# Kernel optimization log

Measured on AMD Instinct MI355X. Metric: run time of the kernel, lower is better.

## Reference

```python
import jax, jax.numpy as jnp
import numpy as np

N, E, F, H, G, C = 50000, 800000, 128, 128, 500, 10
L = 3  # num_conv_layers
EPS = 1e-5


def batch_norm(x, g, b):
    # training-mode BatchNorm1d: biased variance, eps=1e-5
    mu = jnp.mean(x, axis=0)
    var = jnp.var(x, axis=0)
    return (x - mu) * jax.lax.rsqrt(var + EPS) * g + b


def gcn_conv(x, W, bias, src, dst, n):
    # x' = D^{-1/2} (A + I) D^{-1/2} (x W) + bias, edge weights = 1
    xw = x @ W
    loop = jnp.arange(n)
    s = jnp.concatenate([src, loop])  # sources incl. self-loops
    d = jnp.concatenate([dst, loop])  # targets incl. self-loops
    w = jnp.ones(s.shape[0], x.dtype)
    deg = jax.ops.segment_sum(w, s, num_segments=n)
    dinv = jnp.where(deg > 0, jax.lax.rsqrt(deg), 0.0)
    norm = dinv[s] * w * dinv[d]
    msg = xw[s] * norm[:, None]  # gather + scale
    out = jax.ops.segment_sum(msg, d, num_segments=n)  # scatter-add
    return out + bias


def setup_inputs() -> dict:
    key = jax.random.key(0)
    ks = jax.random.split(key, 16)
    x = jax.random.normal(ks[0], (N, F), dtype=jnp.float32)
    edge_index = jax.random.randint(ks[1], (2, E), 0, N, dtype=jnp.int64)
    batch = jnp.sort(jax.random.randint(ks[2], (N,), 0, G, dtype=jnp.int64))
    sF = 1.0 / np.sqrt(F)
    sH = 1.0 / np.sqrt(H)
    return {
        "x": x,
        "edge_index": edge_index,
        "batch": batch,
        "bn_feat_g": jnp.ones((F,), jnp.float32),
        "bn_feat_b": jnp.full((F,), 1e-4, jnp.float32),
        "W_feat": jax.random.normal(ks[3], (F, H), jnp.float32) * sF,
        "bns_conv_g": jnp.ones((L, H), jnp.float32),
        "bns_conv_b": jnp.full((L, H), 1e-4, jnp.float32),
        "W_conv": jax.random.normal(ks[4], (L, H, H), jnp.float32) * sH,
        "b_conv": jnp.zeros((L, H), jnp.float32),
        "bn_fc_g": jnp.ones((H,), jnp.float32),
        "bn_fc_b": jnp.full((H,), 1e-4, jnp.float32),
        "W_lin": jax.random.normal(ks[5], (H, H), jnp.float32) * sH,
        "b_lin": jnp.zeros((H,), jnp.float32),
        "bn_hid_g": jnp.ones((H,), jnp.float32),
        "bn_hid_b": jnp.full((H,), 1e-4, jnp.float32),
        "W_cls": jax.random.normal(ks[6], (H, C), jnp.float32) * sH,
        "b_cls": jnp.zeros((C,), jnp.float32),
    }


def reference(x, edge_index, batch, bn_feat_g, bn_feat_b, W_feat,
              bns_conv_g, bns_conv_b, W_conv, b_conv,
              bn_fc_g, bn_fc_b, W_lin, b_lin,
              bn_hid_g, bn_hid_b, W_cls, b_cls):
    src, dst = edge_index[0], edge_index[1]
    h = batch_norm(x, bn_feat_g, bn_feat_b)
    h = jax.nn.relu(h @ W_feat)  # gfn conv: linear only, no bias/propagation
    for i in range(L):
        h = batch_norm(h, bns_conv_g[i], bns_conv_b[i])
        h = jax.nn.relu(gcn_conv(h, W_conv[i], b_conv[i], src, dst, N))
    h = jax.ops.segment_sum(h, batch, num_segments=G)  # global_add_pool
    h = batch_norm(h, bn_fc_g, bn_fc_b)
    h = jax.nn.relu(h @ W_lin + b_lin)
    h = batch_norm(h, bn_hid_g, bn_hid_b)
    logits = h @ W_cls + b_cls
    return jax.nn.log_softmax(logits, axis=-1)
```

## Files before the change

kernel.cpp:

```cpp
#include <hip/hip_runtime.h>

#define NF 128
#define EPS 1e-5f
#define KELL 64

typedef unsigned short ushort_t;
typedef unsigned int uint_t;

using bf16x8 = __attribute__((ext_vector_type(8))) short;
using f32x4  = __attribute__((ext_vector_type(4))) float;

static __device__ inline ushort_t f2bf(float f) {
    uint_t u = __float_as_uint(f);
    return (ushort_t)((u + 0x7fffu + ((u >> 16) & 1u)) >> 16);
}


__global__ void k_fill_ell(const int* __restrict__ ei, int* __restrict__ scnt,
                           int* __restrict__ dcnt, ushort_t* __restrict__ colx, int E) {
    int e = blockIdx.x * 256 + threadIdx.x;
    if (e < E) {
        int s = ei[e], d = ei[E + e];
        atomicAdd(&scnt[s], 1);
        int pos = atomicAdd(&dcnt[d], 1);
        if (pos < KELL - 1) colx[d * KELL + pos] = (ushort_t)s;
    }
}

__global__ void k_finish(const int* __restrict__ scnt, const int* __restrict__ dcnt,
                         float* __restrict__ dinv, ushort_t* __restrict__ colx,
                         ushort_t* __restrict__ BbSent, int n) {
    int i = blockIdx.x * 256 + threadIdx.x;
    if (i < n) {
        dinv[i] = rsqrtf((float)scnt[i] + 1.0f);
        int dc = min(dcnt[i], KELL - 1);
        ushort_t* row = colx + i * KELL;
        row[dc] = (ushort_t)i;
        int len = (dc + 16) & ~15;
        for (int q = dc + 1; q < len; ++q) row[q] = (ushort_t)n;
    }
    if (blockIdx.x == 0 && threadIdx.x < 64)
        ((uint_t*)BbSent)[threadIdx.x] = 0;
}


__global__ void bn_stats(const float* __restrict__ h, float* __restrict__ stats, int n) {
    int j = threadIdx.x & 127;
    int half = threadIdx.x >> 7;
    float s = 0.f, q = 0.f;
    for (int r = blockIdx.x * 2 + half; r < n; r += gridDim.x * 2) {
        float v = h[r * NF + j];
        s += v;
        q += v * v;
    }
    __shared__ float ls[256], lq[256];
    ls[threadIdx.x] = s; lq[threadIdx.x] = q;
    __syncthreads();
    if (threadIdx.x < 128) {
        atomicAdd(&stats[j], ls[threadIdx.x] + ls[threadIdx.x + 128]);
        atomicAdd(&stats[NF + j], lq[threadIdx.x] + lq[threadIdx.x + 128]);
    }
}


__global__ void pack_w4(const float* __restrict__ W0, const float* __restrict__ W123,
                        ushort_t* __restrict__ Wp) {
    int gidx = blockIdx.x * 256 + threadIdx.x;
    int mat = gidx >> 11, idx = gidx & 2047;
    const float* W = (mat == 0) ? W0 : (W123 + (size_t)(mat - 1) * NF * NF);
    int lane = idx & 63, ct = (idx >> 6) & 7, kc = idx >> 9;
    int m = lane & 15, q = lane >> 4;
    ushort_t o[8];
#pragma unroll
    for (int j = 0; j < 8; ++j)
        o[j] = f2bf(W[(kc * 32 + q * 8 + j) * NF + ct * 16 + m]);
    *(uint4*)&Wp[(size_t)gidx * 8] = *(uint4*)o;
}


#define HSTRIDE 136

__launch_bounds__(256)
__global__ void gemm_mfma(const float* __restrict__ Hh, const ushort_t* __restrict__ Wp,
                          const float* __restrict__ stats, const float* __restrict__ gW,
                          const float* __restrict__ bB, float inv_n,
                          const float* __restrict__ bias, const float* __restrict__ rowscale,
                          float* __restrict__ out, ushort_t* __restrict__ outb,
                          int nrows, int relu, int obf) {
    __shared__ ushort_t hs[64 * HSTRIDE];
    __shared__ float acs[256];
    const int tid = threadIdx.x;
    const int rb = blockIdx.x * 64;

    if (tid < 128) {
        float mean = stats[tid] * inv_n;
        float var = stats[NF + tid] * inv_n - mean * mean;
        float rstd = rsqrtf(var + EPS);
        float a = gW[tid] * rstd;
        acs[tid] = a;
        acs[NF + tid] = bB[tid] - mean * a;
    }
    __syncthreads();
    const float4* ac4 = (const float4*)acs;

#pragma unroll
    for (int p = 0; p < 8; ++p) {
        int idx = p * 256 + tid;
        int r = idx >> 5, k4 = idx & 31;
        int gr = rb + r;
        float4 v = (gr < nrows) ? *(const float4*)&Hh[(size_t)gr * NF + k4 * 4]
                                : make_float4(0.f, 0.f, 0.f, 0.f);
        float4 a4 = ac4[k4], c4 = ac4[32 + k4];
        ushort_t o[4];
        o[0] = f2bf(fmaf(v.x, a4.x, c4.x));
        o[1] = f2bf(fmaf(v.y, a4.y, c4.y));
        o[2] = f2bf(fmaf(v.z, a4.z, c4.z));
        o[3] = f2bf(fmaf(v.w, a4.w, c4.w));
        *(uint2*)&hs[r * HSTRIDE + k4 * 4] = *(uint2*)o;
    }
    __syncthreads();

    const int wave = tid >> 6, lane = tid & 63;
    const int m = lane & 15, q = lane >> 4;
    const ushort_t* arow = &hs[(wave * 16 + m) * HSTRIDE];

    f32x4 acc[8];
#pragma unroll
    for (int ct = 0; ct < 8; ++ct) acc[ct] = (f32x4){0.f, 0.f, 0.f, 0.f};

#pragma unroll
    for (int kc = 0; kc < 4; ++kc) {
        bf16x8 af = *(const bf16x8*)&arow[kc * 32 + q * 8];
        const ushort_t* wp = Wp + kc * 4096 + lane * 8;
#pragma unroll
        for (int ct = 0; ct < 8; ++ct) {
            bf16x8 bfr = *(const bf16x8*)&wp[ct * 512];
            acc[ct] = __builtin_amdgcn_mfma_f32_16x16x32_bf16(af, bfr, acc[ct], 0, 0, 0);
        }
    }

#pragma unroll
    for (int r = 0; r < 4; ++r) {
        int grow = rb + wave * 16 + q * 4 + r;
        if (grow < nrows) {
            float rs = (obf && rowscale) ? rowscale[grow] : 1.0f;
#pragma unroll
            for (int ct = 0; ct < 8; ++ct) {
                int col = ct * 16 + m;
                float v = acc[ct][r] + (bias ? bias[col] : 0.f);
                if (relu) v = fmaxf(v, 0.f);
                if (obf) outb[(size_t)grow * NF + col] = f2bf(v * rs);
                else     out[(size_t)grow * NF + col] = v;
            }
        }
    }
}


__launch_bounds__(256)
__global__ void gemm_bn(const float* __restrict__ Hh, const float* __restrict__ W,
                        const float* __restrict__ stats, const float* __restrict__ gW,
                        const float* __restrict__ bB, float inv_n,
                        const float* __restrict__ bias,
                        float* __restrict__ out, int nrows, int relu) {
    __shared__ float hsb[64][133];
    __shared__ float acs[256];
    const int tid = threadIdx.x;
    const int tx = tid & 15;
    const int ty = tid >> 4;
    const int rb = blockIdx.x * 64;

    if (tid < 128) {
        float mean = stats[tid] * inv_n;
        float var = stats[NF + tid] * inv_n - mean * mean;
        float rstd = rsqrtf(var + EPS);
        float a = gW[tid] * rstd;
        acs[tid] = a;
        acs[NF + tid] = bB[tid] - mean * a;
    }
    __syncthreads();

#pragma unroll 8
    for (int p = 0; p < 32; ++p) {
        int idx = p * 256 + tid;
        int r = idx >> 7, k = idx & 127;
        int gr = rb + r;
        float v = (gr < nrows) ? Hh[(size_t)gr * NF + k] : 0.f;
        hsb[r][k] = fmaf(v, acs[k], acs[NF + k]);
    }
    __syncthreads();

    float acc[4][8];
#pragma unroll
    for (int i = 0; i < 4; ++i)
#pragma unroll
        for (int j = 0; j < 8; ++j) acc[i][j] = 0.f;

    const int c0 = tx * 4, c1 = 64 + tx * 4;
#pragma unroll 4
    for (int k = 0; k < 128; ++k) {
        const float4 b0 = *(const float4*)&W[k * NF + c0];
        const float4 b1 = *(const float4*)&W[k * NF + c1];
#pragma unroll
        for (int i = 0; i < 4; ++i) {
            float a = hsb[ty * 4 + i][k];
            acc[i][0] = fmaf(a, b0.x, acc[i][0]);
            acc[i][1] = fmaf(a, b0.y, acc[i][1]);
            acc[i][2] = fmaf(a, b0.z, acc[i][2]);
            acc[i][3] = fmaf(a, b0.w, acc[i][3]);
            acc[i][4] = fmaf(a, b1.x, acc[i][4]);
            acc[i][5] = fmaf(a, b1.y, acc[i][5]);
            acc[i][6] = fmaf(a, b1.z, acc[i][6]);
            acc[i][7] = fmaf(a, b1.w, acc[i][7]);
        }
    }

#pragma unroll
    for (int i = 0; i < 4; ++i) {
        int gr = rb + ty * 4 + i;
        if (gr < nrows) {
            float o[8];
#pragma unroll
            for (int j = 0; j < 8; ++j) {
                int c = (j < 4) ? (c0 + j) : (c1 + j - 4);
                float v = acc[i][j] + (bias ? bias[c] : 0.f);
                o[j] = relu ? fmaxf(v, 0.f) : v;
            }
            *(float4*)&out[(size_t)gr * NF + c0] = make_float4(o[0], o[1], o[2], o[3]);
            *(float4*)&out[(size_t)gr * NF + c1] = make_float4(o[4], o[5], o[6], o[7]);
        }
    }
}


#define CVT2(u, a, b) { a = __uint_as_float((u) << 16); b = __uint_as_float((u) & 0xffff0000u); }
#define ACC8(q) { float p0, p1, p2, p3, p4, p5, p6, p7;                          \
    CVT2(q.x, p0, p1) CVT2(q.y, p2, p3) CVT2(q.z, p4, p5) CVT2(q.w, p6, p7)      \
    acc[0] += p0; acc[1] += p1; acc[2] += p2; acc[3] += p3;                      \
    acc[4] += p4; acc[5] += p5; acc[6] += p6; acc[7] += p7; }

__launch_bounds__(256)
__global__ void k_aggregate_bf(const ushort_t* __restrict__ xwb, const int* __restrict__ dcnt,
                               const ushort_t* __restrict__ colx, const float* __restrict__ dinv,
                               const float* __restrict__ bias, float* __restrict__ out, int n) {
    int node = blockIdx.x * 16 + (threadIdx.x >> 4);
    int lane = threadIdx.x & 15;
    if (node >= n) return;
    const uint4* __restrict__ xq = (const uint4*)xwb;
    float acc[8];
#pragma unroll
    for (int j = 0; j < 8; ++j) acc[j] = 0.f;
    int dc = min(dcnt[node], KELL - 1);
    int len = (dc + 16) & ~15;
    int e0 = node * KELL;
    for (int e = e0; e < e0 + len; e += 16) {
        uint4 ia = *(const uint4*)&colx[e];
        uint4 ib = *(const uint4*)&colx[e + 8];
        int i0 = ia.x & 0xffff, i1 = ia.x >> 16;
        int i2 = ia.y & 0xffff, i3 = ia.y >> 16;
        int i4 = ia.z & 0xffff, i5 = ia.z >> 16;
        int i6 = ia.w & 0xffff, i7 = ia.w >> 16;
        int i8 = ib.x & 0xffff, i9 = ib.x >> 16;
        int iA = ib.y & 0xffff, iB = ib.y >> 16;
        int iC = ib.z & 0xffff, iD = ib.z >> 16;
        int iE = ib.w & 0xffff, iF = ib.w >> 16;
        uint4 q0 = xq[(size_t)i0 * 16 + lane];
        uint4 q1 = xq[(size_t)i1 * 16 + lane];
        uint4 q2 = xq[(size_t)i2 * 16 + lane];
        uint4 q3 = xq[(size_t)i3 * 16 + lane];
        uint4 q4 = xq[(size_t)i4 * 16 + lane];
        uint4 q5 = xq[(size_t)i5 * 16 + lane];
        uint4 q6 = xq[(size_t)i6 * 16 + lane];
        uint4 q7 = xq[(size_t)i7 * 16 + lane];
        uint4 q8 = xq[(size_t)i8 * 16 + lane];
        uint4 q9 = xq[(size_t)i9 * 16 + lane];
        uint4 qA = xq[(size_t)iA * 16 + lane];
        uint4 qB = xq[(size_t)iB * 16 + lane];
        uint4 qC = xq[(size_t)iC * 16 + lane];
        uint4 qD = xq[(size_t)iD * 16 + lane];
        uint4 qE = xq[(size_t)iE * 16 + lane];
        uint4 qF = xq[(size_t)iF * 16 + lane];
        ACC8(q0) ACC8(q1) ACC8(q2) ACC8(q3)
        ACC8(q4) ACC8(q5) ACC8(q6) ACC8(q7)
        ACC8(q8) ACC8(q9) ACC8(qA) ACC8(qB)
        ACC8(qC) ACC8(qD) ACC8(qE) ACC8(qF)
    }
    float di = dinv[node];
    float4 b0 = *(const float4*)&bias[lane * 8];
    float4 b1 = *(const float4*)&bias[lane * 8 + 4];
    float4 o0, o1;
    o0.x = fmaxf(fmaf(di, acc[0], b0.x), 0.f);
    o0.y = fmaxf(fmaf(di, acc[1], b0.y), 0.f);
    o0.z = fmaxf(fmaf(di, acc[2], b0.z), 0.f);
    o0.w = fmaxf(fmaf(di, acc[3], b0.w), 0.f);
    o1.x = fmaxf(fmaf(di, acc[4], b1.x), 0.f);
    o1.y = fmaxf(fmaf(di, acc[5], b1.y), 0.f);
    o1.z = fmaxf(fmaf(di, acc[6], b1.z), 0.f);
    o1.w = fmaxf(fmaf(di, acc[7], b1.w), 0.f);
    *(float4*)&out[(size_t)node * NF + lane * 8] = o0;
    *(float4*)&out[(size_t)node * NF + lane * 8 + 4] = o1;
}


__global__ void k_pool(const float* __restrict__ h, const int* __restrict__ batch,
                       float* __restrict__ pooled, float* __restrict__ stats, int n) {
    int g = blockIdx.x;
    int t = threadIdx.x;
    int lo = 0, hi = n;
    while (lo < hi) { int m = (lo + hi) >> 1; if (batch[m] < g) lo = m + 1; else hi = m; }
    int start = lo;
    lo = start; hi = n;
    while (lo < hi) { int m = (lo + hi) >> 1; if (batch[m] < g + 1) lo = m + 1; else hi = m; }
    int end = lo;
    float a0 = 0.f, a1 = 0.f, a2 = 0.f, a3 = 0.f;
    int r = start;
    for (; r + 4 <= end; r += 4) {
        a0 += h[(size_t)r * NF + t];
        a1 += h[(size_t)(r + 1) * NF + t];
        a2 += h[(size_t)(r + 2) * NF + t];
        a3 += h[(size_t)(r + 3) * NF + t];
    }
    for (; r < end; ++r) a0 += h[(size_t)r * NF + t];
    float val = (a0 + a1) + (a2 + a3);
    pooled[g * NF + t] = val;
    atomicAdd(&stats[t], val);
    atomicAdd(&stats[NF + t], val * val);
}


__global__ void k_cls(const float* __restrict__ h, const float* __restrict__ stats,
                      const float* __restrict__ gW, const float* __restrict__ bB,
                      float inv_n, const float* __restrict__ Wc,
                      const float* __restrict__ bc, float* __restrict__ out, int C_) {
    __shared__ float hr[128];
    __shared__ float lg[16];
    __shared__ float lse_s;
    int r = blockIdx.x, t = threadIdx.x;
#pragma unroll
    for (int half = 0; half < 2; ++half) {
        int j = t + half * 64;
        float mean = stats[j] * inv_n;
        float var = stats[NF + j] * inv_n - mean * mean;
        float rstd = rsqrtf(var + EPS);
        float a = gW[j] * rstd;
        float c = bB[j] - mean * a;
        hr[j] = fmaf(h[r * NF + j], a, c);
    }
    __syncthreads();
    if (t < C_) {
        float s = bc[t];
        for (int k = 0; k < 128; ++k) s = fmaf(hr[k], Wc[k * C_ + t], s);
        lg[t] = s;
    }
    __syncthreads();
    if (t == 0) {
        float m = -1e30f;
        for (int c = 0; c < C_; ++c) m = fmaxf(m, lg[c]);
        float se = 0.f;
        for (int c = 0; c < C_; ++c) se += expf(lg[c] - m);
        lse_s = m + logf(se);
    }
    __syncthreads();
    if (t < C_) out[r * C_ + t] = lg[t] - lse_s;
}


extern "C" void kernel_launch(void* const* d_in, const int* in_sizes, int n_in,
                              void* d_out, int out_size, void* d_ws, size_t ws_size,
                              hipStream_t stream) {
    const float* x          = (const float*)d_in[0];
    const int*   ei         = (const int*)d_in[1];
    const int*   batch      = (const int*)d_in[2];
    const float* bn_feat_g  = (const float*)d_in[3];
    const float* bn_feat_b  = (const float*)d_in[4];
    const float* W_feat     = (const float*)d_in[5];
    const float* bns_conv_g = (const float*)d_in[6];
    const float* bns_conv_b = (const float*)d_in[7];
    const float* W_conv     = (const float*)d_in[8];
    const float* b_conv     = (const float*)d_in[9];
    const float* bn_fc_g    = (const float*)d_in[10];
    const float* bn_fc_b    = (const float*)d_in[11];
    const float* W_lin      = (const float*)d_in[12];
    const float* b_lin      = (const float*)d_in[13];
    const float* bn_hid_g   = (const float*)d_in[14];
    const float* bn_hid_b   = (const float*)d_in[15];
    const float* W_cls      = (const float*)d_in[16];
    const float* b_cls      = (const float*)d_in[17];
    float* outp = (float*)d_out;

    const int N_ = in_sizes[2];
    const int E_ = in_sizes[1] / 2;
    const int C_ = 10;
    const int G_ = out_size / C_;

    char* wsp = (char*)d_ws;
    auto alloc = [&](size_t bytes) {
        void* p = (void*)wsp;
        wsp += (bytes + 255) & ~(size_t)255;
        return p;
    };
    int*      cnts   = (int*)alloc((size_t)2 * N_ * 4);
    float*    statsA = (float*)alloc(6 * 256 * 4);
    float*    A      = (float*)alloc((size_t)N_ * NF * 4);
    ushort_t* Bb     = (ushort_t*)alloc((size_t)(N_ + 1) * NF * 2);
    float*    dinv   = (float*)alloc((size_t)N_ * 4);
    ushort_t* colx   = (ushort_t*)alloc((size_t)N_ * KELL * 2);
    ushort_t* Wp     = (ushort_t*)alloc((size_t)4 * NF * NF * 2);
    float*    pooled = (float*)alloc((size_t)G_ * NF * 4);
    float*    y2     = (float*)alloc((size_t)G_ * NF * 4);

    int* scnt = cnts;
    int* dcnt = cnts + N_;
    float* st_x  = statsA;
    float* st_f  = statsA + 256;
    float* st_a1 = statsA + 512;
    float* st_a2 = statsA + 768;
    float* st_pl = statsA + 1024;
    float* st_y2 = statsA + 1280;

    int nb_n = (N_ + 255) / 256;
    int nb_e = (E_ + 255) / 256;
    int nb_g = (N_ + 63) / 64;

    size_t cnt_rounded = (((size_t)2 * N_ * 4) + 255) & ~(size_t)255;
    hipMemsetAsync(cnts, 0, cnt_rounded + 6 * 256 * 4, stream);

    k_fill_ell<<<nb_e, 256, 0, stream>>>(ei, scnt, dcnt, colx, E_);
    k_finish<<<nb_n, 256, 0, stream>>>(scnt, dcnt, dinv, colx, Bb + (size_t)N_ * NF, N_);

    pack_w4<<<32, 256, 0, stream>>>(W_feat, W_conv, Wp);

    bn_stats<<<512, 256, 0, stream>>>(x, st_x, N_);
    gemm_mfma<<<nb_g, 256, 0, stream>>>(x, Wp, st_x, bn_feat_g, bn_feat_b, 1.0f / N_,
                                        nullptr, nullptr, A, nullptr, N_, 1, 0);
    bn_stats<<<512, 256, 0, stream>>>(A, st_f, N_);

    float* st_in[3] = {st_f, st_a1, st_a2};
    float* st_out[3] = {st_a1, st_a2, nullptr};
    for (int l = 0; l < 3; ++l) {
        gemm_mfma<<<nb_g, 256, 0, stream>>>(A, Wp + (size_t)(l + 1) * NF * NF,
                                            st_in[l], bns_conv_g + l * NF, bns_conv_b + l * NF,
                                            1.0f / N_, nullptr, dinv, nullptr, Bb, N_, 0, 1);
        k_aggregate_bf<<<(N_ + 15) / 16, 256, 0, stream>>>(Bb, dcnt, colx, dinv,
                                                           b_conv + l * NF, A, N_);
        if (st_out[l])
            bn_stats<<<512, 256, 0, stream>>>(A, st_out[l], N_);
    }

    k_pool<<<G_, 128, 0, stream>>>(A, batch, pooled, st_pl, N_);

    gemm_bn<<<(G_ + 63) / 64, 256, 0, stream>>>(pooled, W_lin, st_pl, bn_fc_g, bn_fc_b,
                                                1.0f / G_, b_lin, y2, G_, 1);
    bn_stats<<<512, 256, 0, stream>>>(y2, st_y2, G_);

    k_cls<<<G_, 64, 0, stream>>>(y2, st_y2, bn_hid_g, bn_hid_b, 1.0f / G_,
                                 W_cls, b_cls, outp, C_);
}
```

Before: 505.5 us.

## Partition ELL construction by block to make neighbor order deterministic

Edge insertion into the ELL adjacency now goes into eight per-partition buckets chosen by block index, each holding up to 16 entries, and a finish pass concatenates them into the final row. This spreads atomic contention on destination counters across partitions and makes neighbor order less dependent on atomic races. It costs a larger memset, an extra intermediate buffer, and a serial merge loop per node. Any partition that receives more than 16 edges for one node silently drops the extras.

```diff
diff --git a/kernel.cpp b/kernel.cpp
--- a/kernel.cpp
+++ b/kernel.cpp
@@ -3,6 +3,8 @@
 #define NF 128
 #define EPS 1e-5f
 #define KELL 64
+#define NPART 8
+#define KP 16
 
 typedef unsigned short ushort_t;
 typedef unsigned int uint_t;
@@ -17,27 +19,38 @@
 
 
 __global__ void k_fill_ell(const int* __restrict__ ei, int* __restrict__ scnt,
-                           int* __restrict__ dcnt, ushort_t* __restrict__ colx, int E) {
+                           int* __restrict__ dcnt8, ushort_t* __restrict__ colx8,
+                           int E, int n) {
     int e = blockIdx.x * 256 + threadIdx.x;
+    int p = blockIdx.x & (NPART - 1);
     if (e < E) {
         int s = ei[e], d = ei[E + e];
         atomicAdd(&scnt[s], 1);
-        int pos = atomicAdd(&dcnt[d], 1);
-        if (pos < KELL - 1) colx[d * KELL + pos] = (ushort_t)s;
-    }
-}
-
-__global__ void k_finish(const int* __restrict__ scnt, const int* __restrict__ dcnt,
-                         float* __restrict__ dinv, ushort_t* __restrict__ colx,
+        int pos = atomicAdd(&dcnt8[p * n + d], 1);
+        if (pos < KP) colx8[((size_t)p * n + d) * KP + pos] = (ushort_t)s;
+    }
+}
+
+__global__ void k_finish(const int* __restrict__ scnt, const int* __restrict__ dcnt8,
+                         int* __restrict__ ucnt, float* __restrict__ dinv,
+                         const ushort_t* __restrict__ colx8, ushort_t* __restrict__ colx,
                          ushort_t* __restrict__ BbSent, int n) {
     int i = blockIdx.x * 256 + threadIdx.x;
     if (i < n) {
         dinv[i] = rsqrtf((float)scnt[i] + 1.0f);
-        int dc = min(dcnt[i], KELL - 1);
-        ushort_t* row = colx + i * KELL;
-        row[dc] = (ushort_t)i;
-        int len = (dc + 16) & ~15;
-        for (int q = dc + 1; q < len; ++q) row[q] = (ushort_t)n;
+        ushort_t* row = colx + (size_t)i * KELL;
+        int w = 0;
+#pragma unroll
+        for (int p = 0; p < NPART; ++p) {
+            int c = dcnt8[p * n + i];
+            if (c > KP) c = KP;
+            const ushort_t* src = colx8 + ((size_t)p * n + i) * KP;
+            for (int j = 0; j < c && w < KELL - 1; ++j) row[w++] = src[j];
+        }
+        ucnt[i] = w;
+        row[w] = (ushort_t)i;
+        int len = (w + 16) & ~15;
+        for (int q = w + 1; q < len; ++q) row[q] = (ushort_t)n;
     }
     if (blockIdx.x == 0 && threadIdx.x < 64)
         ((uint_t*)BbSent)[threadIdx.x] = 0;
@@ -240,7 +253,7 @@
     acc[4] += p4; acc[5] += p5; acc[6] += p6; acc[7] += p7; }
 
 __launch_bounds__(256)
-__global__ void k_aggregate_bf(const ushort_t* __restrict__ xwb, const int* __restrict__ dcnt,
+__global__ void k_aggregate_bf(const ushort_t* __restrict__ xwb, const int* __restrict__ ucnt,
                                const ushort_t* __restrict__ colx, const float* __restrict__ dinv,
                                const float* __restrict__ bias, float* __restrict__ out, int n) {
     int node = blockIdx.x * 16 + (threadIdx.x >> 4);
@@ -250,7 +263,7 @@
     float acc[8];
 #pragma unroll
     for (int j = 0; j < 8; ++j) acc[j] = 0.f;
-    int dc = min(dcnt[node], KELL - 1);
+    int dc = min(ucnt[node], KELL - 1);
     int len = (dc + 16) & ~15;
     int e0 = node * KELL;
     for (int e = e0; e < e0 + len; e += 16) {
@@ -399,18 +412,20 @@
         wsp += (bytes + 255) & ~(size_t)255;
         return p;
     };
-    int*      cnts   = (int*)alloc((size_t)2 * N_ * 4);
+    int*      cnts   = (int*)alloc((size_t)(1 + NPART) * N_ * 4);
     float*    statsA = (float*)alloc(6 * 256 * 4);
     float*    A      = (float*)alloc((size_t)N_ * NF * 4);
     ushort_t* Bb     = (ushort_t*)alloc((size_t)(N_ + 1) * NF * 2);
     float*    dinv   = (float*)alloc((size_t)N_ * 4);
+    int*      ucnt   = (int*)alloc((size_t)N_ * 4);
+    ushort_t* colx8  = (ushort_t*)alloc((size_t)NPART * N_ * KP * 2);
     ushort_t* colx   = (ushort_t*)alloc((size_t)N_ * KELL * 2);
     ushort_t* Wp     = (ushort_t*)alloc((size_t)4 * NF * NF * 2);
     float*    pooled = (float*)alloc((size_t)G_ * NF * 4);
     float*    y2     = (float*)alloc((size_t)G_ * NF * 4);
 
-    int* scnt = cnts;
-    int* dcnt = cnts + N_;
+    int* scnt  = cnts;
+    int* dcnt8 = cnts + N_;
     float* st_x  = statsA;
     float* st_f  = statsA + 256;
     float* st_a1 = statsA + 512;
@@ -422,11 +437,12 @@
     int nb_e = (E_ + 255) / 256;
     int nb_g = (N_ + 63) / 64;
 
-    size_t cnt_rounded = (((size_t)2 * N_ * 4) + 255) & ~(size_t)255;
+    size_t cnt_rounded = (((size_t)(1 + NPART) * N_ * 4) + 255) & ~(size_t)255;
     hipMemsetAsync(cnts, 0, cnt_rounded + 6 * 256 * 4, stream);
 
-    k_fill_ell<<<nb_e, 256, 0, stream>>>(ei, scnt, dcnt, colx, E_);
-    k_finish<<<nb_n, 256, 0, stream>>>(scnt, dcnt, dinv, colx, Bb + (size_t)N_ * NF, N_);
+    k_fill_ell<<<nb_e, 256, 0, stream>>>(ei, scnt, dcnt8, colx8, E_, N_);
+    k_finish<<<nb_n, 256, 0, stream>>>(scnt, dcnt8, ucnt, dinv, colx8, colx,
+                                       Bb + (size_t)N_ * NF, N_);
 
     pack_w4<<<32, 256, 0, stream>>>(W_feat, W_conv, Wp);
 
@@ -441,7 +457,7 @@
         gemm_mfma<<<nb_g, 256, 0, stream>>>(A, Wp + (size_t)(l + 1) * NF * NF,
                                             st_in[l], bns_conv_g + l * NF, bns_conv_b + l * NF,
                                             1.0f / N_, nullptr, dinv, nullptr, Bb, N_, 0, 1);
-        k_aggregate_bf<<<(N_ + 15) / 16, 256, 0, stream>>>(Bb, dcnt, colx, dinv,
+        k_aggregate_bf<<<(N_ + 15) / 16, 256, 0, stream>>>(Bb, ucnt, colx, dinv,
                                                            b_conv + l * NF, A, N_);
         if (st_out[l])
             bn_stats<<<512, 256, 0, stream>>>(A, st_out[l], N_);
```

Result: no change. 514.5 us (+1.8%).
